# Performance work log

Measured on AMD Instinct MI355X. Metric: run time of the kernel, lower is better.

## Reference

```python
import jax, jax.numpy as jnp
import numpy as np

B, S, D, H = 4, 2048, 1024, 16
DH = D // H  # 64
NEG = -1e9


def setup_inputs() -> dict:
    key = jax.random.key(0)
    k1, k2, k3 = jax.random.split(key, 3)
    x = jax.random.normal(k1, (B, S, D), dtype=jnp.float32)
    w_attn = jax.random.normal(k2, (D, 3 * D), dtype=jnp.float32) * 0.02
    b_attn = jnp.zeros((3 * D,), dtype=jnp.float32)
    w_proj = jax.random.normal(k3, (D, D), dtype=jnp.float32) * 0.02
    b_proj = jnp.zeros((D,), dtype=jnp.float32)
    return {"x": x, "w_attn": w_attn, "b_attn": b_attn, "w_proj": w_proj, "b_proj": b_proj}


def reference(x, w_attn, b_attn, w_proj, b_proj):
    # c_attn: fused QKV projection (Conv1D with rf=1 == dense layer)
    qkv = x @ w_attn + b_attn  # [B,S,3D]
    q, k, v = jnp.split(qkv, 3, axis=-1)

    def split_heads(t):  # [B,S,D] -> [B,H,S,DH]
        return t.reshape(B, S, H, DH).transpose(0, 2, 1, 3)

    q, k, v = split_heads(q), split_heads(k), split_heads(v)

    # scaled scores with additive causal mask (as w*b + -1e9*(1-b))
    w = jnp.einsum("bhqd,bhkd->bhqk", q, k) / jnp.sqrt(jnp.float32(DH))
    causal = jnp.tril(jnp.ones((S, S), dtype=w.dtype))[None, None]
    w = w * causal + NEG * (1.0 - causal)
    w = jax.nn.softmax(w, axis=-1)
    # attn_dropout / resid_dropout: p=0 (eval) -> identity

    a = jnp.einsum("bhqk,bhkd->bhqd", w, v)  # [B,H,S,DH]
    a = a.transpose(0, 2, 1, 3).reshape(B, S, D)  # merge heads
    return a @ w_proj + b_proj
```

## Files before the change

### kernel.cpp

```cpp
#include <hip/hip_runtime.h>


typedef short  s8v   __attribute__((ext_vector_type(8)));
typedef float  f32x4 __attribute__((ext_vector_type(4)));
typedef unsigned short u16;
typedef u16    u16x4 __attribute__((ext_vector_type(4)));
typedef unsigned int u32;
typedef u32    u32x2 __attribute__((ext_vector_type(2)));

__device__ __forceinline__ u16 f2b(float f) {
  union { float f; unsigned u; } v; v.f = f;
  unsigned r = v.u + 0x7FFFu + ((v.u >> 16) & 1u);
  return (u16)(r >> 16);
}
__device__ __forceinline__ u32 cvtpk(float lo, float hi) {
  u32 r; asm("v_cvt_pk_bf16_f32 %0, %1, %2" : "=v"(r) : "v"(lo), "v"(hi)); return r;
}

#define QSCALE 0.18033688011112042f

__global__ __launch_bounds__(256) void k_cvt(const float* __restrict__ in,
                                             u16* __restrict__ out, int n4) {
  int t = blockIdx.x * 256 + threadIdx.x;
  if (t < n4) {
    f32x4 f = ((const f32x4*)in)[t];
    u16x4 o;
    o[0] = f2b(f[0]); o[1] = f2b(f[1]); o[2] = f2b(f[2]); o[3] = f2b(f[3]);
    ((u16x4*)out)[t] = o;
  }
}

__global__ __launch_bounds__(256) void k_tr(const float* __restrict__ in,
                                            u16* __restrict__ out, int R, int C) {
  __shared__ float tile[32][33];
  int c0 = blockIdx.x * 32, r0 = blockIdx.y * 32;
  int tx = threadIdx.x, ty = threadIdx.y;
#pragma unroll
  for (int j = 0; j < 4; j++)
    tile[ty + j * 8][tx] = in[(size_t)(r0 + ty + j * 8) * C + c0 + tx];
  __syncthreads();
#pragma unroll
  for (int j = 0; j < 4; j++)
    out[(size_t)(c0 + ty + j * 8) * R + r0 + tx] = f2b(tile[tx][ty + j * 8]);
}

template <int EPI>
__global__ __launch_bounds__(256) void k_gemm(
    const u16* __restrict__ A, const u16* __restrict__ Bt,
    const float* __restrict__ bias,
    u16* __restrict__ qb, u16* __restrict__ kb, u16* __restrict__ vb,
    float* __restrict__ outf, int M, int N, int K) {
  __shared__ u16 lA[128 * 40];
  __shared__ u16 lB[128 * 40];
  const int tid = threadIdx.x;
  const int lane = tid & 63, w = tid >> 6;
  const int wr = (w >> 1) * 64, wc = (w & 1) * 64;
  const int lr = lane & 15, lg = lane >> 4;
  const int m0 = blockIdx.y * 128, n0 = blockIdx.x * 128;

  const int srow = tid >> 1, scol = (tid & 1) * 16;
  const u16* gA = A + (size_t)(m0 + srow) * K + scol;
  const u16* gB = Bt + (size_t)(n0 + srow) * K + scol;

  f32x4 acc[4][4];
  f32x4 zz = {0.f, 0.f, 0.f, 0.f};
#pragma unroll
  for (int m = 0; m < 4; m++)
#pragma unroll
    for (int n = 0; n < 4; n++) acc[m][n] = zz;

  s8v a0 = *(const s8v*)(gA), a1 = *(const s8v*)(gA + 8);
  s8v b0 = *(const s8v*)(gB), b1 = *(const s8v*)(gB + 8);

  const int nk = K / 32;
  for (int kt = 0; kt < nk; ++kt) {
    __syncthreads();
    *(s8v*)&lA[srow * 40 + scol] = a0;
    *(s8v*)&lA[srow * 40 + scol + 8] = a1;
    *(s8v*)&lB[srow * 40 + scol] = b0;
    *(s8v*)&lB[srow * 40 + scol + 8] = b1;
    if (kt + 1 < nk) {
      const u16* nA = gA + (kt + 1) * 32;
      const u16* nB = gB + (kt + 1) * 32;
      a0 = *(const s8v*)(nA); a1 = *(const s8v*)(nA + 8);
      b0 = *(const s8v*)(nB); b1 = *(const s8v*)(nB + 8);
    }
    __syncthreads();
    s8v af[4], bf[4];
#pragma unroll
    for (int m = 0; m < 4; m++)
      af[m] = *(const s8v*)&lA[(wr + m * 16 + lr) * 40 + 8 * lg];
#pragma unroll
    for (int n = 0; n < 4; n++)
      bf[n] = *(const s8v*)&lB[(wc + n * 16 + lr) * 40 + 8 * lg];
#pragma unroll
    for (int m = 0; m < 4; m++)
#pragma unroll
      for (int n = 0; n < 4; n++)
        acc[m][n] = __builtin_amdgcn_mfma_f32_16x16x32_bf16(af[m], bf[n], acc[m][n], 0, 0, 0);
  }

#pragma unroll
  for (int m = 0; m < 4; m++) {
#pragma unroll
    for (int n = 0; n < 4; n++) {
      const int col = n0 + wc + n * 16 + lr;
      const float bb = bias[col];
      const int row0 = m0 + wr + m * 16 + 4 * lg;
      if (EPI == 0) {
        const int which = col >> 10, d = col & 1023, h = d >> 6, dh = d & 63;
        if (which == 2) {
          const int b = row0 >> 11, s = row0 & 2047;
          u16x4 ov;
#pragma unroll
          for (int r = 0; r < 4; r++) ov[r] = f2b(acc[m][n][r] + bb);
          *(u16x4*)(vb + ((size_t)((b * 16 + h) * 64 + dh)) * 2048 + s) = ov;
        } else {
          u16* dst = which == 0 ? qb : kb;
          const float sc = which == 0 ? QSCALE : 1.0f;
#pragma unroll
          for (int r = 0; r < 4; r++) {
            const int row = row0 + r;
            const int b = row >> 11, s = row & 2047;
            dst[(size_t)((b * 16 + h) * 2048 + s) * 64 + dh] = f2b((acc[m][n][r] + bb) * sc);
          }
        }
      } else {
#pragma unroll
        for (int r = 0; r < 4; r++)
          outf[(size_t)(row0 + r) * N + col] = acc[m][n][r] + bb;
      }
    }
  }
}

__global__ __launch_bounds__(256) void k_attn(
    const u16* __restrict__ Q, const u16* __restrict__ K,
    const u16* __restrict__ Vt, u16* __restrict__ O) {
  __shared__ u16 lK[64 * 72];
  __shared__ u16 lV[64 * 72];
  __shared__ u16 lP[4 * 32 * 72];
  const int lin = blockIdx.x;
  const int bh = ((lin & 7) << 3) | (lin >> 6);
  const int pair = (lin >> 3) & 7;
  const int tid = threadIdx.x, lane = tid & 63, w = tid >> 6;
  const int lr = lane & 15, lg = lane >> 4;
  const int sr = tid >> 2, sc = (tid & 3) * 16;
  u16* Pw = &lP[w * (32 * 72)];
  const u16* Kb = K + (size_t)bh * 2048 * 64;
  const u16* Vb = Vt + (size_t)bh * 64 * 2048;
  const int b_ = bh >> 4, h_ = bh & 15;

  s8v k0, k1, v0, v1;
  auto pref = [&](int kv0) {
    const u16* gk = Kb + (size_t)(kv0 + sr) * 64 + sc;
    const u16* gv = Vb + (size_t)sr * 2048 + kv0 + sc;
    k0 = *(const s8v*)gk; k1 = *(const s8v*)(gk + 8);
    v0 = *(const s8v*)gv; v1 = *(const s8v*)(gv + 8);
  };
  pref(0);

  for (int half = 0; half < 2; ++half) {
    const int qt = half == 0 ? pair : 15 - pair;
    const int qbase = qt * 128 + w * 32;
    s8v qf[2][2];
#pragma unroll
    for (int b = 0; b < 2; b++)
#pragma unroll
      for (int h = 0; h < 2; h++)
        qf[b][h] = *(const s8v*)(Q + (size_t)(bh * 2048 + qbase + b * 16 + lr) * 64 + h * 32 + 8 * lg);

    f32x4 accO[4][2];
    f32x4 zz = {0.f, 0.f, 0.f, 0.f};
#pragma unroll
    for (int a = 0; a < 4; a++) { accO[a][0] = zz; accO[a][1] = zz; }
    float mrun[2] = {-1e30f, -1e30f}, lrun[2] = {0.f, 0.f};

    const int ntile = 2 * qt + 2;
    for (int kvt = 0; kvt < ntile; ++kvt) {
      const int kv0 = kvt * 64;
      __syncthreads();
      *(s8v*)&lK[sr * 72 + sc] = k0;
      *(s8v*)&lK[sr * 72 + sc + 8] = k1;
      *(s8v*)&lV[sr * 72 + sc] = v0;
      *(s8v*)&lV[sr * 72 + sc + 8] = v1;
      if (kvt + 1 < ntile) pref((kvt + 1) * 64);
      else if (half == 0) pref(0);
      __syncthreads();

      if (kv0 <= qbase + 31) {
        f32x4 st[4][2];
#pragma unroll
        for (int a = 0; a < 4; a++) {
          s8v af0 = *(const s8v*)&lK[(a * 16 + lr) * 72 + 8 * lg];
          s8v af1 = *(const s8v*)&lK[(a * 16 + lr) * 72 + 32 + 8 * lg];
#pragma unroll
          for (int b = 0; b < 2; b++) {
            f32x4 z = {0.f, 0.f, 0.f, 0.f};
            z = __builtin_amdgcn_mfma_f32_16x16x32_bf16(af0, qf[b][0], z, 0, 0, 0);
            st[a][b] = __builtin_amdgcn_mfma_f32_16x16x32_bf16(af1, qf[b][1], z, 0, 0, 0);
          }
        }
        if (kv0 + 63 > qbase) {
#pragma unroll
          for (int a = 0; a < 4; a++)
#pragma unroll
            for (int b = 0; b < 2; b++)
#pragma unroll
              for (int r = 0; r < 4; r++) {
                const int kk = kv0 + a * 16 + 4 * lg + r;
                const int qq = qbase + b * 16 + lr;
                if (kk > qq) st[a][b][r] = -1e30f;
              }
        }
        float fs[2];
#pragma unroll
        for (int b = 0; b < 2; b++) {
          float mx = st[0][b][0];
#pragma unroll
          for (int a = 0; a < 4; a++)
#pragma unroll
            for (int r = 0; r < 4; r++) mx = fmaxf(mx, st[a][b][r]);
          mx = fmaxf(mx, __shfl_xor(mx, 16));
          mx = fmaxf(mx, __shfl_xor(mx, 32));
          const float mnew = fmaxf(mrun[b], mx);
          const float f = exp2f(mrun[b] - mnew);
          float s = 0.f;
#pragma unroll
          for (int a = 0; a < 4; a++)
#pragma unroll
            for (int r = 0; r < 4; r++) {
              const float e = exp2f(st[a][b][r] - mnew);
              st[a][b][r] = e; s += e;
            }
          s += __shfl_xor(s, 16);
          s += __shfl_xor(s, 32);
          lrun[b] = lrun[b] * f + s;
          mrun[b] = mnew; fs[b] = f;
        }
#pragma unroll
        for (int a = 0; a < 4; a++)
#pragma unroll
          for (int b = 0; b < 2; b++)
#pragma unroll
            for (int r = 0; r < 4; r++) accO[a][b][r] *= fs[b];
#pragma unroll
        for (int b = 0; b < 2; b++)
#pragma unroll
          for (int a = 0; a < 4; a++) {
            u32x2 pk;
            pk[0] = cvtpk(st[a][b][0], st[a][b][1]);
            pk[1] = cvtpk(st[a][b][2], st[a][b][3]);
            *(u32x2*)&Pw[(b * 16 + lr) * 72 + a * 16 + 4 * lg] = pk;
          }
#pragma unroll
        for (int ap = 0; ap < 2; ap++) {
          s8v pf0 = *(const s8v*)&Pw[lr * 72 + ap * 32 + 8 * lg];
          s8v pf1 = *(const s8v*)&Pw[(16 + lr) * 72 + ap * 32 + 8 * lg];
#pragma unroll
          for (int a = 0; a < 4; a++) {
            s8v vf = *(const s8v*)&lV[(a * 16 + lr) * 72 + ap * 32 + 8 * lg];
            accO[a][0] = __builtin_amdgcn_mfma_f32_16x16x32_bf16(vf, pf0, accO[a][0], 0, 0, 0);
            accO[a][1] = __builtin_amdgcn_mfma_f32_16x16x32_bf16(vf, pf1, accO[a][1], 0, 0, 0);
          }
        }
      }
    }
#pragma unroll
    for (int b = 0; b < 2; b++) {
      const float rinv = 1.0f / lrun[b];
      const int qq = qbase + b * 16 + lr;
#pragma unroll
      for (int a = 0; a < 4; a++) {
        u32x2 o;
        o[0] = cvtpk(accO[a][b][0] * rinv, accO[a][b][1] * rinv);
        o[1] = cvtpk(accO[a][b][2] * rinv, accO[a][b][3] * rinv);
        *(u32x2*)(O + (size_t)(b_ * 2048 + qq) * 1024 + h_ * 64 + a * 16 + 4 * lg) = o;
      }
    }
  }
}

extern "C" void kernel_launch(void* const* d_in, const int* in_sizes, int n_in,
                              void* d_out, int out_size, void* d_ws, size_t ws_size,
                              hipStream_t stream) {
  const float* x      = (const float*)d_in[0];
  const float* w_attn = (const float*)d_in[1];
  const float* b_attn = (const float*)d_in[2];
  const float* w_proj = (const float*)d_in[3];
  const float* b_proj = (const float*)d_in[4];
  float* out = (float*)d_out;

  u16* ws  = (u16*)d_ws;
  u16* xb  = ws;
  u16* wTa = xb + 8388608;
  u16* wTp = wTa + 3145728;
  u16* qb  = wTp + 1048576;
  u16* kb  = qb + 8388608;
  u16* vb  = kb + 8388608;

  k_cvt<<<8192, 256, 0, stream>>>(x, xb, 2097152);
  k_tr<<<dim3(96, 32), dim3(32, 8), 0, stream>>>(w_attn, wTa, 1024, 3072);
  k_tr<<<dim3(32, 32), dim3(32, 8), 0, stream>>>(w_proj, wTp, 1024, 1024);
  k_gemm<0><<<dim3(24, 64), 256, 0, stream>>>(xb, wTa, b_attn, qb, kb, vb, nullptr, 8192, 3072, 1024);
  k_attn<<<512, 256, 0, stream>>>(qb, kb, vb, xb);
  k_gemm<1><<<dim3(8, 64), 256, 0, stream>>>(xb, wTp, b_proj, nullptr, nullptr, nullptr, out, 8192, 1024, 1024);
}
```

Baseline: 210.8 us.

## Rewrite attention with 32x32 MFMA, register P, double-buffered KV; GEMM direct-to-LDS loads

```diff
diff --git a/kernel.cpp b/kernel.cpp
--- a/kernel.cpp
+++ b/kernel.cpp
@@ -3,6 +3,7 @@
 
 typedef short  s8v   __attribute__((ext_vector_type(8)));
 typedef float  f32x4 __attribute__((ext_vector_type(4)));
+typedef float  f32x16 __attribute__((ext_vector_type(16)));
 typedef unsigned short u16;
 typedef u16    u16x4 __attribute__((ext_vector_type(4)));
 typedef unsigned int u32;
@@ -15,6 +16,13 @@
 }
 __device__ __forceinline__ u32 cvtpk(float lo, float hi) {
   u32 r; asm("v_cvt_pk_bf16_f32 %0, %1, %2" : "=v"(r) : "v"(lo), "v"(hi)); return r;
+}
+__device__ __forceinline__ void plswap(u32 &d, u32 &s) {
+  asm volatile("v_permlane32_swap_b32 %0, %1" : "+v"(d), "+v"(s));
+}
+__device__ __forceinline__ void gll16(const void* g, void* l) {
+  __builtin_amdgcn_global_load_lds((const __attribute__((address_space(1))) void*)g,
+                                   (__attribute__((address_space(3))) void*)l, 16, 0, 0);
 }
 
 #define QSCALE 0.18033688011112042f
@@ -50,17 +58,18 @@
     const float* __restrict__ bias,
     u16* __restrict__ qb, u16* __restrict__ kb, u16* __restrict__ vb,
     float* __restrict__ outf, int M, int N, int K) {
-  __shared__ u16 lA[128 * 40];
-  __shared__ u16 lB[128 * 40];
+  __shared__ u16 lA[128 * 32];
+  __shared__ u16 lB[128 * 32];
   const int tid = threadIdx.x;
   const int lane = tid & 63, w = tid >> 6;
   const int wr = (w >> 1) * 64, wc = (w & 1) * 64;
   const int lr = lane & 15, lg = lane >> 4;
   const int m0 = blockIdx.y * 128, n0 = blockIdx.x * 128;
 
-  const int srow = tid >> 1, scol = (tid & 1) * 16;
-  const u16* gA = A + (size_t)(m0 + srow) * K + scol;
-  const u16* gB = Bt + (size_t)(n0 + srow) * K + scol;
+  const int crow = lane >> 2;
+  const int ccol = (lane & 3) * 8;
+  const u16* gA = A + (size_t)(m0 + 32 * w + crow) * K + ccol;
+  const u16* gB = Bt + (size_t)(n0 + 32 * w + crow) * K + ccol;
 
   f32x4 acc[4][4];
   f32x4 zz = {0.f, 0.f, 0.f, 0.f};
@@ -69,35 +78,26 @@
 #pragma unroll
     for (int n = 0; n < 4; n++) acc[m][n] = zz;
 
-  s8v a0 = *(const s8v*)(gA), a1 = *(const s8v*)(gA + 8);
-  s8v b0 = *(const s8v*)(gB), b1 = *(const s8v*)(gB + 8);
-
   const int nk = K / 32;
   for (int kt = 0; kt < nk; ++kt) {
-    __syncthreads();
-    *(s8v*)&lA[srow * 40 + scol] = a0;
-    *(s8v*)&lA[srow * 40 + scol + 8] = a1;
-    *(s8v*)&lB[srow * 40 + scol] = b0;
-    *(s8v*)&lB[srow * 40 + scol + 8] = b1;
-    if (kt + 1 < nk) {
-      const u16* nA = gA + (kt + 1) * 32;
-      const u16* nB = gB + (kt + 1) * 32;
-      a0 = *(const s8v*)(nA); a1 = *(const s8v*)(nA + 8);
-      b0 = *(const s8v*)(nB); b1 = *(const s8v*)(nB + 8);
-    }
+    gll16(gA + kt * 32, &lA[w * 1024]);
+    gll16(gA + kt * 32 + 16 * (size_t)K, &lA[w * 1024 + 512]);
+    gll16(gB + kt * 32, &lB[w * 1024]);
+    gll16(gB + kt * 32 + 16 * (size_t)K, &lB[w * 1024 + 512]);
     __syncthreads();
     s8v af[4], bf[4];
 #pragma unroll
     for (int m = 0; m < 4; m++)
-      af[m] = *(const s8v*)&lA[(wr + m * 16 + lr) * 40 + 8 * lg];
+      af[m] = *(const s8v*)&lA[(wr + m * 16 + lr) * 32 + 8 * lg];
 #pragma unroll
     for (int n = 0; n < 4; n++)
-      bf[n] = *(const s8v*)&lB[(wc + n * 16 + lr) * 40 + 8 * lg];
+      bf[n] = *(const s8v*)&lB[(wc + n * 16 + lr) * 32 + 8 * lg];
 #pragma unroll
     for (int m = 0; m < 4; m++)
 #pragma unroll
       for (int n = 0; n < 4; n++)
         acc[m][n] = __builtin_amdgcn_mfma_f32_16x16x32_bf16(af[m], bf[n], acc[m][n], 0, 0, 0);
+    __syncthreads();
   }
 
 #pragma unroll
@@ -134,150 +134,142 @@
   }
 }
 
-__global__ __launch_bounds__(256) void k_attn(
+__global__ __launch_bounds__(256, 3) void k_attn(
     const u16* __restrict__ Q, const u16* __restrict__ K,
     const u16* __restrict__ Vt, u16* __restrict__ O) {
-  __shared__ u16 lK[64 * 72];
-  __shared__ u16 lV[64 * 72];
-  __shared__ u16 lP[4 * 32 * 72];
-  const int lin = blockIdx.x;
-  const int bh = ((lin & 7) << 3) | (lin >> 6);
-  const int pair = (lin >> 3) & 7;
+  __shared__ u16 lKV[2][8192];
+  const int x = blockIdx.x;
+  const int bh = ((x & 7) << 3) | ((x >> 3) & 7);
+  const int qt = 15 - (x >> 6);
   const int tid = threadIdx.x, lane = tid & 63, w = tid >> 6;
-  const int lr = lane & 15, lg = lane >> 4;
-  const int sr = tid >> 2, sc = (tid & 3) * 16;
-  u16* Pw = &lP[w * (32 * 72)];
+  const int l31 = lane & 31, h = lane >> 5;
+  const int qbase = qt * 128 + w * 32;
   const u16* Kb = K + (size_t)bh * 2048 * 64;
   const u16* Vb = Vt + (size_t)bh * 64 * 2048;
+
+  const int skv = tid >> 2;
+  const int ssl = (tid & 3) * 2;
+
+  s8v kR0, kR1, vR0, vR1;
+  auto pref = [&](int kv0) {
+    const u16* gk = Kb + (size_t)(kv0 + skv) * 64 + ssl * 8;
+    const u16* gv = Vb + (size_t)skv * 2048 + kv0 + ssl * 8;
+    kR0 = *(const s8v*)gk; kR1 = *(const s8v*)(gk + 8);
+    vR0 = *(const s8v*)gv; vR1 = *(const s8v*)(gv + 8);
+  };
+  auto stage = [&](int buf) {
+    u16* base = &lKV[buf][0];
+    *(s8v*)&base[(ssl * 64 + (skv ^ ssl)) * 8] = kR0;
+    *(s8v*)&base[((ssl + 1) * 64 + (skv ^ (ssl + 1))) * 8] = kR1;
+    *(s8v*)&base[4096 + (ssl * 64 + (skv ^ ssl)) * 8] = vR0;
+    *(s8v*)&base[4096 + ((ssl + 1) * 64 + (skv ^ (ssl + 1))) * 8] = vR1;
+  };
+
+  s8v qf[4];
+#pragma unroll
+  for (int ks = 0; ks < 4; ks++)
+    qf[ks] = *(const s8v*)(Q + (size_t)(bh * 2048 + qbase + l31) * 64 + ks * 16 + 8 * h);
+
+  f32x16 accO0, accO1;
+#pragma unroll
+  for (int i = 0; i < 16; i++) { accO0[i] = 0.f; accO1[i] = 0.f; }
+  float mrun = -1e30f, lrun = 0.f;
+
+  const int ntile = 2 * qt + 2;
+  pref(0); stage(0);
+  if (ntile > 1) pref(64);
+
+  for (int t = 0; t < ntile; ++t) {
+    const int kv0 = t * 64;
+    __syncthreads();
+    const u16* base = &lKV[t & 1][0];
+
+    if (kv0 <= qbase + 31) {
+      f32x16 st0, st1;
+#pragma unroll
+      for (int i = 0; i < 16; i++) { st0[i] = 0.f; st1[i] = 0.f; }
+#pragma unroll
+      for (int ks = 0; ks < 4; ks++) {
+        const int sl = 2 * ks + h;
+        s8v a0 = *(const s8v*)&base[(sl * 64 + (l31 ^ sl)) * 8];
+        s8v a1 = *(const s8v*)&base[(sl * 64 + ((32 + l31) ^ sl)) * 8];
+        st0 = __builtin_amdgcn_mfma_f32_32x32x16_bf16(a0, qf[ks], st0, 0, 0, 0);
+        st1 = __builtin_amdgcn_mfma_f32_32x32x16_bf16(a1, qf[ks], st1, 0, 0, 0);
+      }
+      if (kv0 + 63 > qbase) {
+        const int dq = qbase + l31 - kv0;
+#pragma unroll
+        for (int r = 0; r < 16; r++) {
+          const int kl = (r & 3) + 8 * (r >> 2) + 4 * h;
+          if (kl > dq) st0[r] = -1e30f;
+          if (kl + 32 > dq) st1[r] = -1e30f;
+        }
+      }
+      float mx = st0[0];
+#pragma unroll
+      for (int r = 1; r < 16; r++) mx = fmaxf(mx, st0[r]);
+#pragma unroll
+      for (int r = 0; r < 16; r++) mx = fmaxf(mx, st1[r]);
+      mx = fmaxf(mx, __shfl_xor(mx, 32));
+      if (!__all(mx <= mrun + 11.0f)) {
+        const float mnew = fmaxf(mrun, mx);
+        const float f = exp2f(mrun - mnew);
+        lrun *= f;
+#pragma unroll
+        for (int r = 0; r < 16; r++) { accO0[r] *= f; accO1[r] *= f; }
+        mrun = mnew;
+      }
+      float s = 0.f;
+#pragma unroll
+      for (int r = 0; r < 16; r++) { st0[r] = exp2f(st0[r] - mrun); s += st0[r]; }
+#pragma unroll
+      for (int r = 0; r < 16; r++) { st1[r] = exp2f(st1[r] - mrun); s += st1[r]; }
+      s += __shfl_xor(s, 32);
+      lrun += s;
+      u32 W0[8], W1[8];
+#pragma unroll
+      for (int a = 0; a < 4; a++) {
+        W0[2 * a]     = cvtpk(st0[4 * a], st0[4 * a + 1]);
+        W0[2 * a + 1] = cvtpk(st0[4 * a + 2], st0[4 * a + 3]);
+        W1[2 * a]     = cvtpk(st1[4 * a], st1[4 * a + 1]);
+        W1[2 * a + 1] = cvtpk(st1[4 * a + 2], st1[4 * a + 3]);
+      }
+#pragma unroll
+      for (int ks = 0; ks < 4; ks++) {
+        const int kp = ks & 1;
+        u32 x0 = (ks < 2) ? W0[4 * kp]     : W1[4 * kp];
+        u32 y0 = (ks < 2) ? W0[4 * kp + 2] : W1[4 * kp + 2];
+        u32 x1 = (ks < 2) ? W0[4 * kp + 1] : W1[4 * kp + 1];
+        u32 y1 = (ks < 2) ? W0[4 * kp + 3] : W1[4 * kp + 3];
+        plswap(x0, y0);
+        plswap(x1, y1);
+        union { u32 u[4]; s8v v; } fb;
+        fb.u[0] = x0; fb.u[1] = x1; fb.u[2] = y0; fb.u[3] = y1;
+        const int sl = 2 * ks + h;
+        s8v va0 = *(const s8v*)&base[4096 + (sl * 64 + (l31 ^ sl)) * 8];
+        s8v va1 = *(const s8v*)&base[4096 + (sl * 64 + ((32 + l31) ^ sl)) * 8];
+        accO0 = __builtin_amdgcn_mfma_f32_32x32x16_bf16(va0, fb.v, accO0, 0, 0, 0);
+        accO1 = __builtin_amdgcn_mfma_f32_32x32x16_bf16(va1, fb.v, accO1, 0, 0, 0);
+      }
+    }
+    if (t + 1 < ntile) {
+      stage((t + 1) & 1);
+      if (t + 2 < ntile) pref((t + 2) * 64);
+    }
+  }
+
   const int b_ = bh >> 4, h_ = bh & 15;
-
-  s8v k0, k1, v0, v1;
-  auto pref = [&](int kv0) {
-    const u16* gk = Kb + (size_t)(kv0 + sr) * 64 + sc;
-    const u16* gv = Vb + (size_t)sr * 2048 + kv0 + sc;
-    k0 = *(const s8v*)gk; k1 = *(const s8v*)(gk + 8);
-    v0 = *(const s8v*)gv; v1 = *(const s8v*)(gv + 8);
-  };
-  pref(0);
-
-  for (int half = 0; half < 2; ++half) {
-    const int qt = half == 0 ? pair : 15 - pair;
-    const int qbase = qt * 128 + w * 32;
-    s8v qf[2][2];
-#pragma unroll
-    for (int b = 0; b < 2; b++)
-#pragma unroll
-      for (int h = 0; h < 2; h++)
-        qf[b][h] = *(const s8v*)(Q + (size_t)(bh * 2048 + qbase + b * 16 + lr) * 64 + h * 32 + 8 * lg);
-
-    f32x4 accO[4][2];
-    f32x4 zz = {0.f, 0.f, 0.f, 0.f};
-#pragma unroll
-    for (int a = 0; a < 4; a++) { accO[a][0] = zz; accO[a][1] = zz; }
-    float mrun[2] = {-1e30f, -1e30f}, lrun[2] = {0.f, 0.f};
-
-    const int ntile = 2 * qt + 2;
-    for (int kvt = 0; kvt < ntile; ++kvt) {
-      const int kv0 = kvt * 64;
-      __syncthreads();
-      *(s8v*)&lK[sr * 72 + sc] = k0;
-      *(s8v*)&lK[sr * 72 + sc + 8] = k1;
-      *(s8v*)&lV[sr * 72 + sc] = v0;
-      *(s8v*)&lV[sr * 72 + sc + 8] = v1;
-      if (kvt + 1 < ntile) pref((kvt + 1) * 64);
-      else if (half == 0) pref(0);
-      __syncthreads();
-
-      if (kv0 <= qbase + 31) {
-        f32x4 st[4][2];
-#pragma unroll
-        for (int a = 0; a < 4; a++) {
-          s8v af0 = *(const s8v*)&lK[(a * 16 + lr) * 72 + 8 * lg];
-          s8v af1 = *(const s8v*)&lK[(a * 16 + lr) * 72 + 32 + 8 * lg];
-#pragma unroll
-          for (int b = 0; b < 2; b++) {
-            f32x4 z = {0.f, 0.f, 0.f, 0.f};
-            z = __builtin_amdgcn_mfma_f32_16x16x32_bf16(af0, qf[b][0], z, 0, 0, 0);
-            st[a][b] = __builtin_amdgcn_mfma_f32_16x16x32_bf16(af1, qf[b][1], z, 0, 0, 0);
-          }
-        }
-        if (kv0 + 63 > qbase) {
-#pragma unroll
-          for (int a = 0; a < 4; a++)
-#pragma unroll
-            for (int b = 0; b < 2; b++)
-#pragma unroll
-              for (int r = 0; r < 4; r++) {
-                const int kk = kv0 + a * 16 + 4 * lg + r;
-                const int qq = qbase + b * 16 + lr;
-                if (kk > qq) st[a][b][r] = -1e30f;
-              }
-        }
-        float fs[2];
-#pragma unroll
-        for (int b = 0; b < 2; b++) {
-          float mx = st[0][b][0];
-#pragma unroll
-          for (int a = 0; a < 4; a++)
-#pragma unroll
-            for (int r = 0; r < 4; r++) mx = fmaxf(mx, st[a][b][r]);
-          mx = fmaxf(mx, __shfl_xor(mx, 16));
-          mx = fmaxf(mx, __shfl_xor(mx, 32));
-          const float mnew = fmaxf(mrun[b], mx);
-          const float f = exp2f(mrun[b] - mnew);
-          float s = 0.f;
-#pragma unroll
-          for (int a = 0; a < 4; a++)
-#pragma unroll
-            for (int r = 0; r < 4; r++) {
-              const float e = exp2f(st[a][b][r] - mnew);
-              st[a][b][r] = e; s += e;
-            }
-          s += __shfl_xor(s, 16);
-          s += __shfl_xor(s, 32);
-          lrun[b] = lrun[b] * f + s;
-          mrun[b] = mnew; fs[b] = f;
-        }
-#pragma unroll
-        for (int a = 0; a < 4; a++)
-#pragma unroll
-          for (int b = 0; b < 2; b++)
-#pragma unroll
-            for (int r = 0; r < 4; r++) accO[a][b][r] *= fs[b];
-#pragma unroll
-        for (int b = 0; b < 2; b++)
-#pragma unroll
-          for (int a = 0; a < 4; a++) {
-            u32x2 pk;
-            pk[0] = cvtpk(st[a][b][0], st[a][b][1]);
-            pk[1] = cvtpk(st[a][b][2], st[a][b][3]);
-            *(u32x2*)&Pw[(b * 16 + lr) * 72 + a * 16 + 4 * lg] = pk;
-          }
-#pragma unroll
-        for (int ap = 0; ap < 2; ap++) {
-          s8v pf0 = *(const s8v*)&Pw[lr * 72 + ap * 32 + 8 * lg];
-          s8v pf1 = *(const s8v*)&Pw[(16 + lr) * 72 + ap * 32 + 8 * lg];
-#pragma unroll
-          for (int a = 0; a < 4; a++) {
-            s8v vf = *(const s8v*)&lV[(a * 16 + lr) * 72 + ap * 32 + 8 * lg];
-            accO[a][0] = __builtin_amdgcn_mfma_f32_16x16x32_bf16(vf, pf0, accO[a][0], 0, 0, 0);
-            accO[a][1] = __builtin_amdgcn_mfma_f32_16x16x32_bf16(vf, pf1, accO[a][1], 0, 0, 0);
-          }
-        }
-      }
-    }
-#pragma unroll
-    for (int b = 0; b < 2; b++) {
-      const float rinv = 1.0f / lrun[b];
-      const int qq = qbase + b * 16 + lr;
-#pragma unroll
-      for (int a = 0; a < 4; a++) {
-        u32x2 o;
-        o[0] = cvtpk(accO[a][b][0] * rinv, accO[a][b][1] * rinv);
-        o[1] = cvtpk(accO[a][b][2] * rinv, accO[a][b][3] * rinv);
-        *(u32x2*)(O + (size_t)(b_ * 2048 + qq) * 1024 + h_ * 64 + a * 16 + 4 * lg) = o;
-      }
-    }
+  const float rinv = 1.0f / lrun;
+  u16* Ob = O + (size_t)(b_ * 2048 + qbase + l31) * 1024 + h_ * 64;
+#pragma unroll
+  for (int a = 0; a < 4; a++) {
+    u32x2 o0, o1;
+    o0[0] = cvtpk(accO0[4 * a] * rinv, accO0[4 * a + 1] * rinv);
+    o0[1] = cvtpk(accO0[4 * a + 2] * rinv, accO0[4 * a + 3] * rinv);
+    o1[0] = cvtpk(accO1[4 * a] * rinv, accO1[4 * a + 1] * rinv);
+    o1[1] = cvtpk(accO1[4 * a + 2] * rinv, accO1[4 * a + 3] * rinv);
+    *(u32x2*)(Ob + 8 * a + 4 * h) = o0;
+    *(u32x2*)(Ob + 32 + 8 * a + 4 * h) = o1;
   }
 }
 
@@ -303,6 +295,6 @@
   k_tr<<<dim3(96, 32), dim3(32, 8), 0, stream>>>(w_attn, wTa, 1024, 3072);
   k_tr<<<dim3(32, 32), dim3(32, 8), 0, stream>>>(w_proj, wTp, 1024, 1024);
   k_gemm<0><<<dim3(24, 64), 256, 0, stream>>>(xb, wTa, b_attn, qb, kb, vb, nullptr, 8192, 3072, 1024);
-  k_attn<<<512, 256, 0, stream>>>(qb, kb, vb, xb);
+  k_attn<<<1024, 256, 0, stream>>>(qb, kb, vb, xb);
   k_gemm<1><<<dim3(8, 64), 256, 0, stream>>>(xb, wTp, b_proj, nullptr, nullptr, nullptr, out, 8192, 1024, 1024);
 }
```

After: 195.5 us. 7.2% less time.
